# Optimization experiments

Hardware: AMD Instinct MI355X
Metric: run time of the kernel (lower is better)

The kernel has to match this reference:

```python
import math
import jax, jax.numpy as jnp
import numpy as np

B, S, D, H, DH, R, V = 8, 1024, 1024, 8, 512, 36, 32002  # DH = d_model//2, HD = h*DH = 4096
HD = H * DH
LN_EPS = 1e-5


def setup_inputs() -> dict:
    key = jax.random.key(0)
    ks = jax.random.split(key, 16)

    def n(k, shp, std=0.02):
        return jax.random.normal(k, shp, jnp.float32) * std

    pre_words = jax.random.randint(ks[0], (B, S), 0, V)
    img_features = jax.random.normal(ks[1], (B, R, D), jnp.float32)
    exp_embed = n(ks[2], (V, D)).at[0].set(0.0)  # padding_idx=0
    # id2visual table: sparse nonneg rows over 36 regions; zero rows -> textual tokens
    id2vis = (jax.random.uniform(ks[3], (V, R)) < 0.05).astype(jnp.float32)
    # stacked params for 2 transformer layers; weights stored (in, out) so y = x @ W + b
    wq = n(ks[4], (2, D, HD)); bq = jnp.zeros((2, HD), jnp.float32)
    wk = n(ks[5], (2, D, HD)); bk = jnp.zeros((2, HD), jnp.float32)
    wv = n(ks[6], (2, D, HD)); bv = jnp.zeros((2, HD), jnp.float32)
    wo = n(ks[7], (2, HD, D)); bo = jnp.zeros((2, D), jnp.float32)
    w1 = n(ks[8], (2, D, D)); b1 = jnp.zeros((2, D), jnp.float32)
    w2 = n(ks[9], (2, D, D)); b2 = jnp.zeros((2, D), jnp.float32)
    ln1_g = jnp.ones((2, D), jnp.float32); ln1_b = jnp.zeros((2, D), jnp.float32)
    ln2_g = jnp.ones((2, D), jnp.float32); ln2_b = jnp.zeros((2, D), jnp.float32)
    return dict(pre_words=pre_words, img_features=img_features, exp_embed=exp_embed,
                id2vis=id2vis, wq=wq, bq=bq, wk=wk, bk=bk, wv=wv, bv=bv, wo=wo, bo=bo,
                w1=w1, b1=b1, w2=w2, b2=b2, ln1_g=ln1_g, ln1_b=ln1_b, ln2_g=ln2_g, ln2_b=ln2_b)


def _layer_norm(x, g, b):
    m = x.mean(-1, keepdims=True)
    v = ((x - m) ** 2).mean(-1, keepdims=True)
    return (x - m) / jnp.sqrt(v + LN_EPS) * g + b


def _softmax_one(x):
    # shifted-denominator softmax: exp(x - max) / (1 + sum exp(x - max))
    x = x - x.max(-1, keepdims=True)
    e = jnp.exp(x)
    return e / (1.0 + e.sum(-1, keepdims=True))


def reference(pre_words, img_features, exp_embed, id2vis, wq, bq, wk, bk, wv, bv,
              wo, bo, w1, b1, w2, b2, ln1_g, ln1_b, ln2_g, ln2_b):
    # token embedding: textual (masked to 0 where a visual row exists) + visual bmm
    te = exp_embed[pre_words]                       # (B,S,D)
    vids = id2vis[pre_words]                        # (B,S,R)
    word_mask = vids.sum(-1, keepdims=True) != 0    # (B,S,1)
    ve = jnp.einsum('bsr,brd->bsd', vids, img_features)
    x = jnp.where(word_mask, 0.0, te) + ve          # (B,S,D)

    scale = 1.0 / math.sqrt(DH)
    for i in range(2):  # two structurally identical transformer layers
        h = _layer_norm(x, ln1_g[i], ln1_b[i])
        q = (h @ wq[i] + bq[i]).reshape(B, S, H, DH).transpose(0, 2, 1, 3)
        k = (h @ wk[i] + bk[i]).reshape(B, S, H, DH).transpose(0, 2, 1, 3)
        v = (h @ wv[i] + bv[i]).reshape(B, S, H, DH).transpose(0, 2, 1, 3)
        attn = _softmax_one(jnp.einsum('bhqd,bhkd->bhqk', q, k) * scale)  # (B,H,S,S)
        o = jnp.einsum('bhqk,bhkd->bhqd', attn, v)
        o = o.transpose(0, 2, 1, 3).reshape(B, S, HD)
        x = x + (o @ wo[i] + bo[i])
        f = _layer_norm(x, ln2_g[i], ln2_b[i])
        f = jax.nn.gelu(f @ w1[i] + b1[i], approximate=False) @ w2[i] + b2[i]
        x = x + f
    return x
```

## Files before the change

### kernel.cpp

```cpp
#include <hip/hip_runtime.h>


using u16 = unsigned short;
typedef __attribute__((ext_vector_type(8))) short bf16x8;
typedef __attribute__((ext_vector_type(4))) float f32x4;

__device__ __forceinline__ float b2f(u16 u) {
  union { unsigned int i; float f; } v; v.i = ((unsigned int)u) << 16; return v.f;
}
__device__ __forceinline__ u16 f2b(float f) {
  union { float f; unsigned int i; } v; v.f = f;
  unsigned int i = v.i;
  return (u16)((i + 0x7FFFu + ((i >> 16) & 1u)) >> 16);
}
__device__ __forceinline__ float gelu_f(float x) {
  return 0.5f * x * (1.f + erff(x * 0.70710678118654752f));
}
__device__ __forceinline__ void async16(void* lds, const void* g) {
  __builtin_amdgcn_global_load_lds((const __attribute__((address_space(1))) void*)g,
                                   (__attribute__((address_space(3))) void*)lds, 16, 0, 0);
}
__device__ __forceinline__ void storeC(float* p, float v) { *p = v; }
__device__ __forceinline__ void storeC(u16* p, float v) { *p = f2b(v); }

__global__ __launch_bounds__(256) void embed_k(
    const int* __restrict__ words, const float* __restrict__ img,
    const float* __restrict__ emb, const float* __restrict__ id2v,
    float* __restrict__ x)
{
  __shared__ float vs[36];
  int tok = blockIdx.x, b = tok >> 10, t = threadIdx.x;
  int wd = words[tok];
  if (t < 36) vs[t] = id2v[(size_t)wd * 36 + t];
  __syncthreads();
  bool any = false;
#pragma unroll
  for (int r = 0; r < 36; ++r) any = any || (vs[r] != 0.f);
#pragma unroll
  for (int i = 0; i < 4; ++i) {
    int d = t + (i << 8);
    float acc = 0.f;
    for (int r = 0; r < 36; ++r) {
      float vv = vs[r];
      if (vv != 0.f) acc += vv * img[((size_t)(b * 36 + r) << 10) + d];
    }
    float te = any ? 0.f : emb[((size_t)wd << 10) + d];
    x[((size_t)tok << 10) + d] = te + acc;
  }
}

__global__ __launch_bounds__(256) void ln_k(
    const float* __restrict__ x, u16* __restrict__ out,
    const float* __restrict__ g, const float* __restrict__ bb)
{
  __shared__ float red[4];
  int row = blockIdx.x, t = threadIdx.x;
  const float* xr = x + ((size_t)row << 10);
  float v[4], s = 0.f;
#pragma unroll
  for (int i = 0; i < 4; ++i) { v[i] = xr[t + (i << 8)]; s += v[i]; }
#pragma unroll
  for (int o = 32; o; o >>= 1) s += __shfl_xor(s, o, 64);
  if ((t & 63) == 0) red[t >> 6] = s;
  __syncthreads();
  s = red[0] + red[1] + red[2] + red[3];
  float mean = s * 0.0009765625f;
  float q = 0.f;
#pragma unroll
  for (int i = 0; i < 4; ++i) { float d = v[i] - mean; q += d * d; }
  __syncthreads();
#pragma unroll
  for (int o = 32; o; o >>= 1) q += __shfl_xor(q, o, 64);
  if ((t & 63) == 0) red[t >> 6] = q;
  __syncthreads();
  q = red[0] + red[1] + red[2] + red[3];
  float rstd = rsqrtf(q * 0.0009765625f + 1e-5f);
  u16* orow = out + ((size_t)row << 10);
#pragma unroll
  for (int i = 0; i < 4; ++i) {
    int d = t + (i << 8);
    orow[d] = f2b((v[i] - mean) * rstd * g[d] + bb[d]);
  }
}

__global__ __launch_bounds__(256) void sm_k(const u16* __restrict__ S, u16* __restrict__ P)
{
  __shared__ float red[4];
  size_t row = blockIdx.x;
  int t = threadIdx.x;
  const u16* sr = S + (row << 10);
  ushort4 sv = *(const ushort4*)(sr + (t << 2));
  float v[4] = { b2f(sv.x), b2f(sv.y), b2f(sv.z), b2f(sv.w) };
  float m = fmaxf(fmaxf(v[0], v[1]), fmaxf(v[2], v[3]));
#pragma unroll
  for (int o = 32; o; o >>= 1) m = fmaxf(m, __shfl_xor(m, o, 64));
  if ((t & 63) == 0) red[t >> 6] = m;
  __syncthreads();
  m = fmaxf(fmaxf(red[0], red[1]), fmaxf(red[2], red[3]));
  float e[4], s = 0.f;
#pragma unroll
  for (int i = 0; i < 4; ++i) { e[i] = __expf(v[i] - m); s += e[i]; }
  __syncthreads();
#pragma unroll
  for (int o = 32; o; o >>= 1) s += __shfl_xor(s, o, 64);
  if ((t & 63) == 0) red[t >> 6] = s;
  __syncthreads();
  s = red[0] + red[1] + red[2] + red[3];
  float inv = 1.f / (1.f + s);
  ushort4 pv;
  pv.x = f2b(e[0] * inv); pv.y = f2b(e[1] * inv);
  pv.z = f2b(e[2] * inv); pv.w = f2b(e[3] * inv);
  *(ushort4*)(P + (row << 10) + (t << 2)) = pv;
}

__global__ __launch_bounds__(256) void tr_k(
    const float* __restrict__ src, u16* __restrict__ dst, int ls, int ld)
{
  __shared__ u16 tile[64][65];
  int c0 = blockIdx.x << 6, r0 = blockIdx.y << 6;
  int tx = threadIdx.x & 63, ty0 = threadIdx.x >> 6;
#pragma unroll
  for (int i = 0; i < 16; ++i) {
    int ty = (ty0 << 4) + i;
    tile[ty][tx] = f2b(src[(size_t)(r0 + ty) * ls + (c0 + tx)]);
  }
  __syncthreads();
#pragma unroll
  for (int i = 0; i < 16; ++i) {
    int ty = (ty0 << 4) + i;
    dst[(size_t)(c0 + ty) * ld + (r0 + tx)] = tile[tx][ty];
  }
}

template <typename CT, int ACT, int BIAS, int RESID>
__global__ __launch_bounds__(512, 1) void gemm8p(
    const u16* __restrict__ A, const u16* __restrict__ Bt,
    CT* __restrict__ C, const float* __restrict__ bias,
    const float* __restrict__ resid,
    int M, int N, int K, int lda, int ldb, int ldc, float scale,
    int zbase, int zdiv, int ga, int gb, int gc,
    long long aS1, long long aS2, long long bS1, long long bS2,
    long long cS1, long long cS2)
{
  __shared__ u16 lA[2][256 * 64];
  __shared__ u16 lB[2][256 * 64];
  const int nwg = gridDim.x * gridDim.y;
  const int id = blockIdx.y * gridDim.x + blockIdx.x;
  const int qq = nwg >> 3, rr8 = nwg & 7;
  const int xcd = id & 7, off = id >> 3;
  const int swz = (xcd < rr8 ? xcd * (qq + 1) : rr8 * (qq + 1) + (xcd - rr8) * qq) + off;
  const int bx = swz % gridDim.x, by = swz / gridDim.x;

  long long lz = blockIdx.z;
  long long gz = zbase + lz;
  long long zA = ga ? gz : lz, zB = gb ? gz : lz, zC = gc ? gz : lz;
  size_t aOff = (size_t)((zA / zdiv) * aS1 + (zA % zdiv) * aS2);
  size_t bOff = (size_t)((zB / zdiv) * bS1 + (zB % zdiv) * bS2);
  size_t cOff = (size_t)((zC / zdiv) * cS1 + (zC % zdiv) * cS2);
  const int m0 = by << 8, n0 = bx << 8;
  const int tid = threadIdx.x, lane = tid & 63, w = tid >> 6;
  const int wm = w >> 2, wn = w & 3;
  const int srow8 = lane >> 3;
  const int schunk = (lane & 7) ^ srow8;
  const int fr = lane & 15, hi = lane >> 4;

  f32x4 acc[8][4];
#pragma unroll
  for (int mi = 0; mi < 8; ++mi)
#pragma unroll
    for (int ni = 0; ni < 4; ++ni) acc[mi][ni] = 0.f;

  const u16* Ab = A + aOff;
  const u16* Bb = Bt + bOff;

  auto STAGE = [&](int buf, int k0) {
#pragma unroll
    for (int s = 0; s < 4; ++s) {
      const int rb = (s << 6) + (w << 3);
      async16(&lA[buf][rb << 6], Ab + (size_t)(m0 + rb + srow8) * lda + (k0 + (schunk << 3)));
      async16(&lB[buf][rb << 6], Bb + (size_t)(n0 + rb + srow8) * ldb + (k0 + (schunk << 3)));
    }
  };

  const int nt = K >> 6;
  STAGE(0, 0);
  STAGE(1, 64);
  for (int t = 0; t < nt; ++t) {
    const int cur = t & 1;
    if (t + 1 < nt) asm volatile("s_waitcnt vmcnt(8)" ::: "memory");
    else            asm volatile("s_waitcnt vmcnt(0)" ::: "memory");
    __builtin_amdgcn_s_barrier();
    __builtin_amdgcn_sched_barrier(0);
#pragma unroll
    for (int ks = 0; ks < 2; ++ks) {
      const int q = (ks << 2) + hi;
      bf16x8 a8[8], b8[4];
#pragma unroll
      for (int mi = 0; mi < 8; ++mi) {
        const int R = (wm << 7) + (mi << 4) + fr;
        a8[mi] = *(const bf16x8*)&lA[cur][(R << 6) + ((q ^ (R & 7)) << 3)];
      }
#pragma unroll
      for (int ni = 0; ni < 4; ++ni) {
        const int R = (wn << 6) + (ni << 4) + fr;
        b8[ni] = *(const bf16x8*)&lB[cur][(R << 6) + ((q ^ (R & 7)) << 3)];
      }
      __builtin_amdgcn_s_setprio(1);
#pragma unroll
      for (int mi = 0; mi < 8; ++mi)
#pragma unroll
        for (int ni = 0; ni < 4; ++ni)
          acc[mi][ni] = __builtin_amdgcn_mfma_f32_16x16x32_bf16(a8[mi], b8[ni], acc[mi][ni], 0, 0, 0);
      __builtin_amdgcn_s_setprio(0);
    }
    if (t + 2 < nt) {
      asm volatile("s_waitcnt lgkmcnt(0)" ::: "memory");
      __builtin_amdgcn_s_barrier();
      __builtin_amdgcn_sched_barrier(0);
      STAGE(cur, (t + 2) << 6);
    }
  }

  const int r4 = hi << 2, cc = fr;
#pragma unroll
  for (int mi = 0; mi < 8; ++mi) {
#pragma unroll
    for (int ni = 0; ni < 4; ++ni) {
      const int col = n0 + (wn << 6) + (ni << 4) + cc;
      float bcol = 0.f;
      if (BIAS == 1) bcol = bias[col];
#pragma unroll
      for (int j = 0; j < 4; ++j) {
        const int row = m0 + (wm << 7) + (mi << 4) + r4 + j;
        float v = acc[mi][ni][j] * scale + bcol;
        if (BIAS == 2) v += bias[row];
        if (ACT == 1) v = gelu_f(v);
        const size_t idx = cOff + (size_t)row * ldc + col;
        if (RESID) v += resid[idx];
        storeC(&C[idx], v);
      }
    }
  }
}

template <typename CT, int ACT, int BIAS, int RESID, int BN>
__global__ __launch_bounds__(256, 4) void gemm_t(
    const u16* __restrict__ A, const u16* __restrict__ Bt,
    CT* __restrict__ C, const float* __restrict__ bias,
    const float* __restrict__ resid,
    int M, int N, int K, int lda, int ldb, int ldc, float scale,
    int zbase, int zdiv, int ga, int gb, int gc,
    long long aS1, long long aS2, long long bS1, long long bS2,
    long long cS1, long long cS2)
{
  constexpr int NACC = BN / 32;
  __shared__ u16 lA[128 * 64];
  __shared__ u16 lB[BN * 64];
  const int nwg = gridDim.x * gridDim.y;
  const int id = blockIdx.y * gridDim.x + blockIdx.x;
  const int qq = nwg >> 3, rr8 = nwg & 7;
  const int xcd = id & 7, off = id >> 3;
  const int swz = (xcd < rr8 ? xcd * (qq + 1) : rr8 * (qq + 1) + (xcd - rr8) * qq) + off;
  const int bx = swz % gridDim.x, by = swz / gridDim.x;

  long long lz = blockIdx.z;
  long long gz = zbase + lz;
  long long zA = ga ? gz : lz, zB = gb ? gz : lz, zC = gc ? gz : lz;
  size_t aOff = (size_t)((zA / zdiv) * aS1 + (zA % zdiv) * aS2);
  size_t bOff = (size_t)((zB / zdiv) * bS1 + (zB % zdiv) * bS2);
  size_t cOff = (size_t)((zC / zdiv) * cS1 + (zC % zdiv) * cS2);
  const int m0 = by << 7, n0 = bx * BN;
  const int tid = threadIdx.x, lane = tid & 63, w = tid >> 6;
  const int wm = w >> 1, wn = w & 1;
  const int srow8 = lane >> 3;
  const int schunk = (lane & 7) ^ srow8;
  const int fr = lane & 15, hi = lane >> 4;

  f32x4 acc[4][NACC];
#pragma unroll
  for (int mi = 0; mi < 4; ++mi)
#pragma unroll
    for (int ni = 0; ni < NACC; ++ni) acc[mi][ni] = 0.f;

  const u16* Ab = A + aOff;
  const u16* Bb = Bt + bOff;

  for (int k0 = 0; k0 < K; k0 += 64) {
#pragma unroll
    for (int s = 0; s < 4; ++s) {
      const int rb = (s << 5) + (w << 3);
      async16(&lA[rb << 6], Ab + (size_t)(m0 + rb + srow8) * lda + (k0 + (schunk << 3)));
    }
#pragma unroll
    for (int s = 0; s < BN / 32; ++s) {
      const int rb = (s << 5) + (w << 3);
      async16(&lB[rb << 6], Bb + (size_t)(n0 + rb + srow8) * ldb + (k0 + (schunk << 3)));
    }
    __syncthreads();
#pragma unroll
    for (int ks = 0; ks < 2; ++ks) {
      const int q = (ks << 2) + hi;
      bf16x8 a8[4], b8[NACC];
#pragma unroll
      for (int mi = 0; mi < 4; ++mi) {
        const int R = (wm << 6) + (mi << 4) + fr;
        a8[mi] = *(const bf16x8*)&lA[(R << 6) + ((q ^ (R & 7)) << 3)];
      }
#pragma unroll
      for (int ni = 0; ni < NACC; ++ni) {
        const int R = wn * (BN / 2) + (ni << 4) + fr;
        b8[ni] = *(const bf16x8*)&lB[(R << 6) + ((q ^ (R & 7)) << 3)];
      }
#pragma unroll
      for (int mi = 0; mi < 4; ++mi)
#pragma unroll
        for (int ni = 0; ni < NACC; ++ni)
          acc[mi][ni] = __builtin_amdgcn_mfma_f32_16x16x32_bf16(a8[mi], b8[ni], acc[mi][ni], 0, 0, 0);
    }
    __syncthreads();
  }

  const int r4 = hi << 2, cc = fr;
#pragma unroll
  for (int mi = 0; mi < 4; ++mi) {
#pragma unroll
    for (int ni = 0; ni < NACC; ++ni) {
      const int col = n0 + wn * (BN / 2) + (ni << 4) + cc;
      float bcol = 0.f;
      if (BIAS == 1) bcol = bias[col];
#pragma unroll
      for (int j = 0; j < 4; ++j) {
        const int row = m0 + (wm << 6) + (mi << 4) + r4 + j;
        float v = acc[mi][ni][j] * scale + bcol;
        if (BIAS == 2) v += bias[row];
        if (ACT == 1) v = gelu_f(v);
        const size_t idx = cOff + (size_t)row * ldc + col;
        if (RESID) v += resid[idx];
        storeC(&C[idx], v);
      }
    }
  }
}

extern "C" void kernel_launch(void* const* d_in, const int* in_sizes, int n_in,
                              void* d_out, int out_size, void* d_ws, size_t ws_size,
                              hipStream_t stream)
{
  (void)in_sizes; (void)n_in; (void)out_size;
  const int*   pre_words = (const int*)d_in[0];
  const float* img  = (const float*)d_in[1];
  const float* emb  = (const float*)d_in[2];
  const float* id2v = (const float*)d_in[3];
  const float* wq = (const float*)d_in[4];  const float* bq = (const float*)d_in[5];
  const float* wk = (const float*)d_in[6];  const float* bk = (const float*)d_in[7];
  const float* wv = (const float*)d_in[8];  const float* bv = (const float*)d_in[9];
  const float* wo = (const float*)d_in[10]; const float* bo = (const float*)d_in[11];
  const float* w1 = (const float*)d_in[12]; const float* b1 = (const float*)d_in[13];
  const float* w2 = (const float*)d_in[14]; const float* b2 = (const float*)d_in[15];
  const float* ln1g = (const float*)d_in[16]; const float* ln1b = (const float*)d_in[17];
  const float* ln2g = (const float*)d_in[18]; const float* ln2b = (const float*)d_in[19];

  const size_t FIXED = 88080384 + (size_t)(1 << 16);
  int g = 1;
  for (int c = 8; c >= 1; c >>= 1)
    if (FIXED + (size_t)c * 33554432 + 4194304 <= ws_size) { g = c; break; }
  int nc = 1;
  int ncmax = 8 * g > 32 ? 32 : 8 * g;
  for (int c = ncmax; c >= 1; c >>= 1)
    if (FIXED + (size_t)g * 33554432 + (size_t)c * 4194304 <= ws_size) { nc = c; break; }

  char* p = (char*)d_ws;
  auto alloc = [&](size_t bytes) -> void* {
    void* r = (void*)p; p += (bytes + 255) & ~(size_t)255; return r;
  };
  float* x  = (float*)alloc((size_t)8192 * 1024 * 4);
  u16* h    = (u16*)alloc((size_t)8192 * 1024 * 2);
  u16* Qg   = (u16*)alloc((size_t)g * 1024 * 4096 * 2);
  u16* Og   = (u16*)alloc((size_t)g * 1024 * 4096 * 2);
  u16* ff   = Qg;
  u16* Kg   = (u16*)alloc((size_t)g * 1024 * 4096 * 2);
  u16* Vtg  = (u16*)alloc((size_t)g * 4096 * 1024 * 2);
  u16* wqt  = (u16*)alloc((size_t)4096 * 1024 * 2);
  u16* wkt  = (u16*)alloc((size_t)4096 * 1024 * 2);
  u16* wvt  = (u16*)alloc((size_t)4096 * 1024 * 2);
  u16* wot  = (u16*)alloc((size_t)1024 * 4096 * 2);
  u16* w1t  = (u16*)alloc((size_t)1024 * 1024 * 2);
  u16* w2t  = (u16*)alloc((size_t)1024 * 1024 * 2);
  u16* Sc   = (u16*)alloc((size_t)nc << 21);
  u16* Pp   = (u16*)alloc((size_t)nc << 21);

  embed_k<<<8192, 256, 0, stream>>>(pre_words, img, emb, id2v, x);

  const float qk_scale = 0.044194173824159216f;
  for (int L = 0; L < 2; ++L) {
    const float* WQ = wq + (size_t)L * 1024 * 4096;
    const float* WK = wk + (size_t)L * 1024 * 4096;
    const float* WV = wv + (size_t)L * 1024 * 4096;
    const float* WO = wo + (size_t)L * 4096 * 1024;
    const float* W1 = w1 + (size_t)L * 1024 * 1024;
    const float* W2 = w2 + (size_t)L * 1024 * 1024;

    tr_k<<<dim3(64, 16), 256, 0, stream>>>(WQ, wqt, 4096, 1024);
    tr_k<<<dim3(64, 16), 256, 0, stream>>>(WK, wkt, 4096, 1024);
    tr_k<<<dim3(64, 16), 256, 0, stream>>>(WV, wvt, 4096, 1024);
    tr_k<<<dim3(16, 64), 256, 0, stream>>>(WO, wot, 1024, 4096);
    tr_k<<<dim3(16, 16), 256, 0, stream>>>(W1, w1t, 1024, 1024);
    tr_k<<<dim3(16, 16), 256, 0, stream>>>(W2, w2t, 1024, 1024);

    ln_k<<<8192, 256, 0, stream>>>(x, h, ln1g + L * 1024, ln1b + L * 1024);

    for (int g0 = 0; g0 < 8; g0 += g) {
      const u16* hg = h + (size_t)g0 * 1048576;
      const int Mg = 1024 * g;
      gemm8p<u16, 0, 1, 0><<<dim3(16, Mg >> 8), 512, 0, stream>>>(
          hg, wqt, Qg, bq + (size_t)L * 4096, nullptr,
          Mg, 4096, 1024, 1024, 1024, 4096, 1.f,
          0, 1, 0, 0, 0, 0, 0, 0, 0, 0, 0);
      gemm8p<u16, 0, 1, 0><<<dim3(16, Mg >> 8), 512, 0, stream>>>(
          hg, wkt, Kg, bk + (size_t)L * 4096, nullptr,
          Mg, 4096, 1024, 1024, 1024, 4096, 1.f,
          0, 1, 0, 0, 0, 0, 0, 0, 0, 0, 0);
      gemm8p<u16, 0, 2, 0><<<dim3(4, 16, g), 512, 0, stream>>>(
          wvt, h, Vtg, bv + (size_t)L * 4096, nullptr,
          4096, 1024, 1024, 1024, 1024, 1024, 1.f,
          g0, 1, 0, 1, 0, 0, 0, 1048576LL, 0, 4194304LL, 0);
      for (int c0 = 0; c0 < 8 * g; c0 += nc) {
        gemm8p<u16, 0, 0, 0><<<dim3(4, 4, nc), 512, 0, stream>>>(
            Qg, Kg, Sc, nullptr, nullptr,
            1024, 1024, 512, 4096, 4096, 1024, qk_scale,
            c0, 8, 1, 1, 0,
            4194304LL, 512LL, 4194304LL, 512LL, 8388608LL, 1048576LL);
        sm_k<<<nc << 10, 256, 0, stream>>>(Sc, Pp);
        gemm8p<u16, 0, 0, 0><<<dim3(2, 4, nc), 512, 0, stream>>>(
            Pp, Vtg, Og, nullptr, nullptr,
            1024, 512, 1024, 1024, 1024, 4096, 1.f,
            c0, 8, 0, 1, 1,
            8388608LL, 1048576LL, 4194304LL, 524288LL, 4194304LL, 512LL);
      }
      gemm_t<float, 0, 1, 1, 64><<<dim3(16, Mg >> 7), 256, 0, stream>>>(
          Og, wot, x + (size_t)g0 * 1048576, bo + (size_t)L * 1024,
          x + (size_t)g0 * 1048576,
          Mg, 1024, 4096, 4096, 4096, 1024, 1.f,
          0, 1, 0, 0, 0, 0, 0, 0, 0, 0, 0);
    }

    ln_k<<<8192, 256, 0, stream>>>(x, h, ln2g + L * 1024, ln2b + L * 1024);

    gemm_t<u16, 1, 1, 0, 64><<<dim3(16, 64), 256, 0, stream>>>(
        h, w1t, ff, b1 + (size_t)L * 1024, nullptr,
        8192, 1024, 1024, 1024, 1024, 1024, 1.f,
        0, 1, 0, 0, 0, 0, 0, 0, 0, 0, 0);
    float* cdst = (L == 1) ? (float*)d_out : x;
    gemm_t<float, 0, 1, 1, 64><<<dim3(16, 64), 256, 0, stream>>>(
        ff, w2t, cdst, b2 + (size_t)L * 1024, x,
        8192, 1024, 1024, 1024, 1024, 1024, 1.f,
        0, 1, 0, 0, 0, 0, 0, 0, 0, 0, 0);
  }
}
```

Measured before the change: 1.496 ms.

## Interleave split global-to-LDS staging with MFMA phases in GEMM main loop

Splits each K-tile's global-to-LDS staging into B and two halves of A, and issues them across four compute phases inside the main loop instead of one block after compute. The A rows 1/3 for the next tile are loaded later, and the vmcnt wait threshold is adjusted to match. The MFMA loop is reordered so each phase handles two M sub-tiles over both k-steps, with B fragments held for the whole tile. This aims to hide global load latency behind MFMA work, at the cost of more barriers per tile and tricky buffer hazards.

```diff
diff --git a/kernel.cpp b/kernel.cpp
--- a/kernel.cpp
+++ b/kernel.cpp
@@ -173,51 +173,82 @@
   const u16* Ab = A + aOff;
   const u16* Bb = Bt + bOff;
 
-  auto STAGE = [&](int buf, int k0) {
+  auto ST_B = [&](int buf, int k0) {
 #pragma unroll
     for (int s = 0; s < 4; ++s) {
       const int rb = (s << 6) + (w << 3);
+      async16(&lB[buf][rb << 6], Bb + (size_t)(n0 + rb + srow8) * ldb + (k0 + (schunk << 3)));
+    }
+  };
+  auto ST_A02 = [&](int buf, int k0) {
+#pragma unroll
+    for (int s = 0; s < 4; s += 2) {
+      const int rb = (s << 6) + (w << 3);
       async16(&lA[buf][rb << 6], Ab + (size_t)(m0 + rb + srow8) * lda + (k0 + (schunk << 3)));
-      async16(&lB[buf][rb << 6], Bb + (size_t)(n0 + rb + srow8) * ldb + (k0 + (schunk << 3)));
     }
   };
+  auto ST_A13 = [&](int buf, int k0) {
+#pragma unroll
+    for (int s = 1; s < 4; s += 2) {
+      const int rb = (s << 6) + (w << 3);
+      async16(&lA[buf][rb << 6], Ab + (size_t)(m0 + rb + srow8) * lda + (k0 + (schunk << 3)));
+    }
+  };
 
   const int nt = K >> 6;
-  STAGE(0, 0);
-  STAGE(1, 64);
+  ST_B(0, 0); ST_A02(0, 0); ST_A13(0, 0);
+  ST_B(1, 64); ST_A02(1, 64);
+
   for (int t = 0; t < nt; ++t) {
     const int cur = t & 1;
-    if (t + 1 < nt) asm volatile("s_waitcnt vmcnt(8)" ::: "memory");
+    if (t + 1 < nt) asm volatile("s_waitcnt vmcnt(6)" ::: "memory");
     else            asm volatile("s_waitcnt vmcnt(0)" ::: "memory");
     __builtin_amdgcn_s_barrier();
     __builtin_amdgcn_sched_barrier(0);
-#pragma unroll
-    for (int ks = 0; ks < 2; ++ks) {
-      const int q = (ks << 2) + hi;
-      bf16x8 a8[8], b8[4];
-#pragma unroll
-      for (int mi = 0; mi < 8; ++mi) {
-        const int R = (wm << 7) + (mi << 4) + fr;
-        a8[mi] = *(const bf16x8*)&lA[cur][(R << 6) + ((q ^ (R & 7)) << 3)];
-      }
-#pragma unroll
-      for (int ni = 0; ni < 4; ++ni) {
-        const int R = (wn << 6) + (ni << 4) + fr;
-        b8[ni] = *(const bf16x8*)&lB[cur][(R << 6) + ((q ^ (R & 7)) << 3)];
-      }
+
+    bf16x8 b8[4][2];
+    const int kt2 = (t + 2) << 6;
+#pragma unroll
+    for (int p = 0; p < 4; ++p) {
+      if (p == 0) {
+#pragma unroll
+        for (int ni = 0; ni < 4; ++ni)
+#pragma unroll
+          for (int ks = 0; ks < 2; ++ks) {
+            const int R = (wn << 6) + (ni << 4) + fr;
+            const int q = (ks << 2) + hi;
+            b8[ni][ks] = *(const bf16x8*)&lB[cur][(R << 6) + ((q ^ (R & 7)) << 3)];
+          }
+      }
+      bf16x8 a8[2][2];
+#pragma unroll
+      for (int i = 0; i < 2; ++i)
+#pragma unroll
+        for (int ks = 0; ks < 2; ++ks) {
+          const int mi = (p << 1) + i;
+          const int R = (wm << 7) + (mi << 4) + fr;
+          const int q = (ks << 2) + hi;
+          a8[i][ks] = *(const bf16x8*)&lA[cur][(R << 6) + ((q ^ (R & 7)) << 3)];
+        }
+      if (p == 0) { if (t + 1 < nt) ST_A13(cur ^ 1, (t + 1) << 6); }
+      else if (p == 1) { if (t + 2 < nt) ST_B(cur, kt2); }
+      else if (p == 2) { if (t + 2 < nt) ST_A02(cur, kt2); }
+      __builtin_amdgcn_s_barrier();
+      asm volatile("s_waitcnt lgkmcnt(0)" ::: "memory");
+      __builtin_amdgcn_sched_barrier(0);
       __builtin_amdgcn_s_setprio(1);
 #pragma unroll
-      for (int mi = 0; mi < 8; ++mi)
+      for (int i = 0; i < 2; ++i)
 #pragma unroll
         for (int ni = 0; ni < 4; ++ni)
-          acc[mi][ni] = __builtin_amdgcn_mfma_f32_16x16x32_bf16(a8[mi], b8[ni], acc[mi][ni], 0, 0, 0);
+#pragma unroll
+          for (int ks = 0; ks < 2; ++ks)
+            acc[(p << 1) + i][ni] =
+                __builtin_amdgcn_mfma_f32_16x16x32_bf16(a8[i][ks], b8[ni][ks],
+                                                        acc[(p << 1) + i][ni], 0, 0, 0);
       __builtin_amdgcn_s_setprio(0);
-    }
-    if (t + 2 < nt) {
-      asm volatile("s_waitcnt lgkmcnt(0)" ::: "memory");
       __builtin_amdgcn_s_barrier();
       __builtin_amdgcn_sched_barrier(0);
-      STAGE(cur, (t + 2) << 6);
     }
   }
 
```

After: 1.497 ms. Within noise of the previous version (+0.1%).
